# Kernel tuning notes

Measured on AMD Instinct MI355X. Metric: run time of the kernel, lower is better.

The kernel has to match this reference:

```python
import jax, jax.numpy as jnp
import numpy as np

D = 256  # input_dim
B = 2048

def setup_inputs() -> dict:
    key = jax.random.key(0)
    ks = jax.random.split(key, 6)
    x = jax.random.normal(ks[0], (B, D), dtype=jnp.float32)
    offsets = jax.random.normal(ks[1], (D,), dtype=jnp.float32)
    coeff0 = jax.random.normal(ks[2], (), dtype=jnp.float32)
    coeff1 = jax.random.normal(ks[3], (D,), dtype=jnp.float32)
    coeff2 = jax.random.normal(ks[4], (D, D), dtype=jnp.float32)
    coeff3 = jax.random.normal(ks[5], (D, D, D), dtype=jnp.float32)
    return {"x": x, "offsets": offsets, "coeff0": coeff0, "coeff1": coeff1,
            "coeff2": coeff2, "coeff3": coeff3}

def reference(x, offsets, coeff0, coeff1, coeff2, coeff3):
    # Truncated Taylor series around learned offsets: out[b] = c0 + sum_i <coeff_i, rel^{\otimes i}>[b]
    rel = x - offsets  # (B, D)
    out = coeff0  # scalar, broadcasts to (B,)
    for c in (coeff1, coeff2, coeff3):
        # contract one mode of the rank-i coefficient with rel at a time
        t = jnp.einsum('...d,bd->b...', c, rel)  # (B, D^{i-1})
        while t.ndim > 1:
            t = jnp.einsum('b...d,bd->b...', t, rel)
        out = out + t  # (B,)
    return out
```

## Files before the change

kernel.cpp:

```cpp
#include <hip/hip_runtime.h>
#include <hip/hip_bf16.h>

#define DD 256
#define BB 2048
#define BM 128
#define BN 64
#define NTILE ((DD * DD) / BM)
#define NSTAGE (BB / BN)

typedef __bf16 bf16x8 __attribute__((ext_vector_type(8)));
typedef float  f32x4  __attribute__((ext_vector_type(4)));

#define AS1 __attribute__((address_space(1)))
#define AS3 __attribute__((address_space(3)))

__device__ __forceinline__ unsigned short f2bf(float f) {
    unsigned int u = __float_as_uint(f);
    return (unsigned short)((u + 0x7FFFu + ((u >> 16) & 1u)) >> 16);
}
__device__ __forceinline__ float bf2f(unsigned short s) {
    return __uint_as_float(((unsigned int)s) << 16);
}
__device__ __forceinline__ void async_cp16(const void* g, void* l) {
    __builtin_amdgcn_global_load_lds((const AS1 unsigned int*)g,
                                     (AS3 unsigned int*)l, 16, 0, 0);
}

__global__ void prep_all(const float* __restrict__ x, const float* __restrict__ offsets,
                         const float* __restrict__ c0, const float* __restrict__ c1,
                         float* __restrict__ rel_f32, unsigned short* __restrict__ rel_bf16,
                         float* __restrict__ out) {
    const int tid = threadIdx.x, wave = tid >> 6, lane = tid & 63;
    const float4 o4  = *(const float4*)(offsets + lane * 4);
    const float4 c14 = *(const float4*)(c1 + lane * 4);
#pragma unroll
    for (int i = 0; i < 2; ++i) {
        const int b = blockIdx.x * 8 + wave * 2 + i;
        const float4 x4 = *(const float4*)(x + (size_t)b * DD + lane * 4);
        float4 r;
        r.x = x4.x - o4.x; r.y = x4.y - o4.y; r.z = x4.z - o4.z; r.w = x4.w - o4.w;
        *(float4*)(rel_f32 + (size_t)b * DD + lane * 4) = r;
        ushort4 rb;
        rb.x = f2bf(r.x); rb.y = f2bf(r.y); rb.z = f2bf(r.z); rb.w = f2bf(r.w);
        *(ushort4*)(rel_bf16 + (size_t)b * DD + lane * 4) = rb;
        float s = r.x * c14.x + r.y * c14.y + r.z * c14.z + r.w * c14.w;
        s += __shfl_xor(s, 1);  s += __shfl_xor(s, 2);  s += __shfl_xor(s, 4);
        s += __shfl_xor(s, 8);  s += __shfl_xor(s, 16); s += __shfl_xor(s, 32);
        if (lane == 0) out[b] = c0[0] + s;
    }
}

__global__ __launch_bounds__(512, 4) void taylor3(
    const float* __restrict__ c3, const float* __restrict__ c2,
    const float* __restrict__ rel_f32, const unsigned short* __restrict__ rel_bf16,
    float* __restrict__ partial)
{
    __shared__ unsigned short Bs[2][BN * DD];
    __shared__ float relI[BB];
    __shared__ float c2row[BM];
    __shared__ float colsum[2][4][BN];

    const int tile = blockIdx.x;
    const int i_t   = tile >> 1;
    const int jbase = (tile & 1) << 7;
    const int tid  = threadIdx.x;
    const int wave = tid >> 6;
    const int lane = tid & 63;
    const int wm = wave & 3, wn = wave >> 2;
    const int lrow = lane & 15, quad = lane >> 4;

#pragma unroll
    for (int k = 0; k < 4; ++k) {
        const int b = tid + k * 512;
        relI[b] = rel_f32[(size_t)b * DD + i_t];
    }
    if (tid < BM) c2row[tid] = c2[i_t * DD + jbase + tid];

    bf16x8 afr[8][2];
    {
        const float* abase = c3 + (size_t)tile * BM * DD;
#pragma unroll
        for (int mt = 0; mt < 2; ++mt) {
            const int row = wm * 32 + mt * 16 + lrow;
            const float* p = abase + (size_t)row * DD + quad * 8;
#pragma unroll
            for (int ks = 0; ks < 8; ++ks) {
                float4 f0 = *(const float4*)(p + ks * 32);
                float4 f1 = *(const float4*)(p + ks * 32 + 4);
                union { unsigned short u[8]; bf16x8 v; } cv;
                cv.u[0] = f2bf(f0.x); cv.u[1] = f2bf(f0.y);
                cv.u[2] = f2bf(f0.z); cv.u[3] = f2bf(f0.w);
                cv.u[4] = f2bf(f1.x); cv.u[5] = f2bf(f1.y);
                cv.u[6] = f2bf(f1.z); cv.u[7] = f2bf(f1.w);
                afr[ks][mt] = cv.v;
            }
        }
    }

    auto stage = [&](int nb, int buf) {
        const int b0 = nb * BN;
#pragma unroll
        for (int c = 0; c < 4; ++c) {
            const int r0 = c * 16 + wave * 2;
            const int row = r0 + (lane >> 5);
            const int g = (lane & 31) ^ (row & 7);
            const unsigned short* src = rel_bf16 + (size_t)(b0 + row) * DD + g * 8;
            async_cp16(src, &Bs[buf][r0 * DD]);
        }
    };

    stage(0, 0);
    int prev_b0 = -1;

    for (int nb = 0; nb < NSTAGE; ++nb) {
        const int cur = nb & 1;
        const int b0 = nb * BN;
        __syncthreads();
        if (nb + 1 < NSTAGE) stage(nb + 1, cur ^ 1);

        if (prev_b0 >= 0 && tid < BN) {
            const float v = colsum[cur ^ 1][0][tid] + colsum[cur ^ 1][1][tid]
                          + colsum[cur ^ 1][2][tid] + colsum[cur ^ 1][3][tid];
            partial[(size_t)tile * BB + prev_b0 + tid] = relI[prev_b0 + tid] * v;
        }

        f32x4 acc[2][2];
#pragma unroll
        for (int mt = 0; mt < 2; ++mt)
#pragma unroll
            for (int nt = 0; nt < 2; ++nt)
                acc[mt][nt] = (f32x4){0.f, 0.f, 0.f, 0.f};

#pragma unroll
        for (int ks = 0; ks < 8; ++ks) {
            bf16x8 bfr[2];
#pragma unroll
            for (int nt = 0; nt < 2; ++nt) {
                const int col = wn * 32 + nt * 16 + lrow;
                const int g = (ks * 4 + quad) ^ (col & 7);
                bfr[nt] = *(const bf16x8*)(&Bs[cur][col * DD + g * 8]);
            }
#pragma unroll
            for (int mt = 0; mt < 2; ++mt)
#pragma unroll
                for (int nt = 0; nt < 2; ++nt)
                    acc[mt][nt] = __builtin_amdgcn_mfma_f32_16x16x32_bf16(
                        afr[ks][mt], bfr[nt], acc[mt][nt], 0, 0, 0);
        }

        float sv[2];
#pragma unroll
        for (int nt = 0; nt < 2; ++nt) {
            const int col = wn * 32 + nt * 16 + lrow;
            float s = 0.f;
#pragma unroll
            for (int mt = 0; mt < 2; ++mt) {
                const int el = wm * 32 + mt * 16 + quad * 4;
                const int e  = jbase + el;
                const int g  = (e >> 3) ^ (col & 7);
                const ushort4 rj = *(const ushort4*)(&Bs[cur][col * DD + g * 8 + (e & 7)]);
                const float4 c2r = *(const float4*)(&c2row[el]);
                s += (acc[mt][nt][0] + c2r.x) * bf2f(rj.x);
                s += (acc[mt][nt][1] + c2r.y) * bf2f(rj.y);
                s += (acc[mt][nt][2] + c2r.z) * bf2f(rj.z);
                s += (acc[mt][nt][3] + c2r.w) * bf2f(rj.w);
            }
            s += __shfl_xor(s, 16, 64);
            s += __shfl_xor(s, 32, 64);
            sv[nt] = s;
        }
        if (lane < 32) colsum[cur][wm][wn * 32 + lane] = sv[lane >> 4];
        prev_b0 = b0;
    }
    __syncthreads();
    if (tid < BN) {
        const float v = colsum[1][0][tid] + colsum[1][1][tid]
                      + colsum[1][2][tid] + colsum[1][3][tid];
        partial[(size_t)tile * BB + prev_b0 + tid] = relI[prev_b0 + tid] * v;
    }
}

__global__ void reduce_partial(const float* __restrict__ partial, float* __restrict__ out) {
    __shared__ f32x4 red[256];
    const int t = threadIdx.x;
    const int g = blockIdx.x * 4 + (t & 3);
    const int slice = t >> 2;
    f32x4 s = (f32x4){0.f, 0.f, 0.f, 0.f};
    for (int r = slice * 8; r < slice * 8 + 8; ++r)
        s += *(const f32x4*)(partial + (size_t)r * BB + g * 4);
    red[t] = s; __syncthreads();
    if (t < 128) red[t] += red[t + 128]; __syncthreads();
    if (t < 64)  red[t] += red[t + 64];  __syncthreads();
    if (t < 32)  red[t] += red[t + 32];  __syncthreads();
    if (t < 16)  red[t] += red[t + 16];  __syncthreads();
    if (t < 8)   red[t] += red[t + 8];   __syncthreads();
    if (t < 4) {
        const f32x4 v = red[t] + red[t + 4];
        float4* op = (float4*)(out + (size_t)(blockIdx.x * 4 + t) * 4);
        float4 o = *op;
        o.x += v[0]; o.y += v[1]; o.z += v[2]; o.w += v[3];
        *op = o;
    }
}

extern "C" void kernel_launch(void* const* d_in, const int* in_sizes, int n_in,
                              void* d_out, int out_size, void* d_ws, size_t ws_size,
                              hipStream_t stream) {
    const float* x       = (const float*)d_in[0];
    const float* offsets = (const float*)d_in[1];
    const float* c0      = (const float*)d_in[2];
    const float* c1      = (const float*)d_in[3];
    const float* c2      = (const float*)d_in[4];
    const float* c3      = (const float*)d_in[5];
    float* out = (float*)d_out;

    char* ws = (char*)d_ws;
    float* rel_f32 = (float*)ws;
    unsigned short* rel_bf16 = (unsigned short*)(ws + (size_t)BB * DD * 4);
    float* partial = (float*)(ws + (size_t)BB * DD * 6);

    prep_all<<<BB / 8, 256, 0, stream>>>(x, offsets, c0, c1, rel_f32, rel_bf16, out);
    taylor3<<<NTILE, 512, 0, stream>>>(c3, c2, rel_f32, rel_bf16, partial);
    reduce_partial<<<128, 256, 0, stream>>>(partial, out);
}
```

Before: 221.9 us.

## Split K dimension across wave pairs instead of N in taylor3 MFMA tiling

Each wave pair now splits the 256-wide contraction dimension in halves and covers all 64 batch columns, instead of splitting the columns. This halves the per-wave A fragment registers (afr 8x2 to 4x2) while doubling accumulators and B fragment loads per k-step. The c2 term is added only by the first K half, and colsum grows to 8 partial rows that are summed before writing partial. It trades register pressure and A reuse for more LDS reads of B and a larger cross-wave reduction.

```diff
diff --git a/kernel.cpp b/kernel.cpp
--- a/kernel.cpp
+++ b/kernel.cpp
@@ -58,7 +58,7 @@
     __shared__ unsigned short Bs[2][BN * DD];
     __shared__ float relI[BB];
     __shared__ float c2row[BM];
-    __shared__ float colsum[2][4][BN];
+    __shared__ float colsum[2][8][BN];
 
     const int tile = blockIdx.x;
     const int i_t   = tile >> 1;
@@ -66,7 +66,7 @@
     const int tid  = threadIdx.x;
     const int wave = tid >> 6;
     const int lane = tid & 63;
-    const int wm = wave & 3, wn = wave >> 2;
+    const int wm = wave & 3, wk = wave >> 2;
     const int lrow = lane & 15, quad = lane >> 4;
 
 #pragma unroll
@@ -76,15 +76,15 @@
     }
     if (tid < BM) c2row[tid] = c2[i_t * DD + jbase + tid];
 
-    bf16x8 afr[8][2];
+    bf16x8 afr[4][2];
     {
         const float* abase = c3 + (size_t)tile * BM * DD;
 #pragma unroll
         for (int mt = 0; mt < 2; ++mt) {
             const int row = wm * 32 + mt * 16 + lrow;
-            const float* p = abase + (size_t)row * DD + quad * 8;
-#pragma unroll
-            for (int ks = 0; ks < 8; ++ks) {
+            const float* p = abase + (size_t)row * DD + wk * 128 + quad * 8;
+#pragma unroll
+            for (int ks = 0; ks < 4; ++ks) {
                 float4 f0 = *(const float4*)(p + ks * 32);
                 float4 f1 = *(const float4*)(p + ks * 32 + 4);
                 union { unsigned short u[8]; bf16x8 v; } cv;
@@ -119,39 +119,41 @@
         if (nb + 1 < NSTAGE) stage(nb + 1, cur ^ 1);
 
         if (prev_b0 >= 0 && tid < BN) {
-            const float v = colsum[cur ^ 1][0][tid] + colsum[cur ^ 1][1][tid]
-                          + colsum[cur ^ 1][2][tid] + colsum[cur ^ 1][3][tid];
+            float v = 0.f;
+#pragma unroll
+            for (int w = 0; w < 8; ++w) v += colsum[cur ^ 1][w][tid];
             partial[(size_t)tile * BB + prev_b0 + tid] = relI[prev_b0 + tid] * v;
         }
 
-        f32x4 acc[2][2];
+        f32x4 acc[2][4];
 #pragma unroll
         for (int mt = 0; mt < 2; ++mt)
 #pragma unroll
-            for (int nt = 0; nt < 2; ++nt)
+            for (int nt = 0; nt < 4; ++nt)
                 acc[mt][nt] = (f32x4){0.f, 0.f, 0.f, 0.f};
 
 #pragma unroll
-        for (int ks = 0; ks < 8; ++ks) {
-            bf16x8 bfr[2];
-#pragma unroll
-            for (int nt = 0; nt < 2; ++nt) {
-                const int col = wn * 32 + nt * 16 + lrow;
-                const int g = (ks * 4 + quad) ^ (col & 7);
+        for (int ks = 0; ks < 4; ++ks) {
+            const int glog = wk * 16 + ks * 4 + quad;
+            bf16x8 bfr[4];
+#pragma unroll
+            for (int nt = 0; nt < 4; ++nt) {
+                const int col = nt * 16 + lrow;
+                const int g = glog ^ (col & 7);
                 bfr[nt] = *(const bf16x8*)(&Bs[cur][col * DD + g * 8]);
             }
 #pragma unroll
             for (int mt = 0; mt < 2; ++mt)
 #pragma unroll
-                for (int nt = 0; nt < 2; ++nt)
+                for (int nt = 0; nt < 4; ++nt)
                     acc[mt][nt] = __builtin_amdgcn_mfma_f32_16x16x32_bf16(
                         afr[ks][mt], bfr[nt], acc[mt][nt], 0, 0, 0);
         }
 
-        float sv[2];
-#pragma unroll
-        for (int nt = 0; nt < 2; ++nt) {
-            const int col = wn * 32 + nt * 16 + lrow;
+        float sv[4];
+#pragma unroll
+        for (int nt = 0; nt < 4; ++nt) {
+            const int col = nt * 16 + lrow;
             float s = 0.f;
 #pragma unroll
             for (int mt = 0; mt < 2; ++mt) {
@@ -159,23 +161,32 @@
                 const int e  = jbase + el;
                 const int g  = (e >> 3) ^ (col & 7);
                 const ushort4 rj = *(const ushort4*)(&Bs[cur][col * DD + g * 8 + (e & 7)]);
-                const float4 c2r = *(const float4*)(&c2row[el]);
-                s += (acc[mt][nt][0] + c2r.x) * bf2f(rj.x);
-                s += (acc[mt][nt][1] + c2r.y) * bf2f(rj.y);
-                s += (acc[mt][nt][2] + c2r.z) * bf2f(rj.z);
-                s += (acc[mt][nt][3] + c2r.w) * bf2f(rj.w);
+                float c2x = 0.f, c2y = 0.f, c2z = 0.f, c2w = 0.f;
+                if (wk == 0) {
+                    const float4 c2r = *(const float4*)(&c2row[el]);
+                    c2x = c2r.x; c2y = c2r.y; c2z = c2r.z; c2w = c2r.w;
+                }
+                s += (acc[mt][nt][0] + c2x) * bf2f(rj.x);
+                s += (acc[mt][nt][1] + c2y) * bf2f(rj.y);
+                s += (acc[mt][nt][2] + c2z) * bf2f(rj.z);
+                s += (acc[mt][nt][3] + c2w) * bf2f(rj.w);
             }
             s += __shfl_xor(s, 16, 64);
             s += __shfl_xor(s, 32, 64);
             sv[nt] = s;
         }
-        if (lane < 32) colsum[cur][wm][wn * 32 + lane] = sv[lane >> 4];
+        {
+            const float v01 = (quad & 1) ? sv[1] : sv[0];
+            const float v23 = (quad & 1) ? sv[3] : sv[2];
+            colsum[cur][wave][lane] = (quad & 2) ? v23 : v01;
+        }
         prev_b0 = b0;
     }
     __syncthreads();
     if (tid < BN) {
-        const float v = colsum[1][0][tid] + colsum[1][1][tid]
-                      + colsum[1][2][tid] + colsum[1][3][tid];
+        float v = 0.f;
+#pragma unroll
+        for (int w = 0; w < 8; ++w) v += colsum[1][w][tid];
         partial[(size_t)tile * BB + prev_b0 + tid] = relI[prev_b0 + tid] * v;
     }
 }
```

Measured after the change: 191.4 us. 13.7% less time.
